# Optimization experiments

Measured on AMD Instinct MI355X. Metric: run time of the kernel, lower is better.

The kernel has to match this reference:

```python
import jax, jax.numpy as jnp
import numpy as np

B = 16384       # batch
H = 512         # hidden_size
OUT = 4         # output_size (== GRU input_size)
FF = 2048       # MLP hidden width
HORIZON = 5     # prediction_horizon


def setup_inputs() -> dict:
    key = jax.random.key(0)
    ks = jax.random.split(key, 12)
    s = 0.05
    f32 = jnp.float32
    return {
        "predicted_values": jax.random.normal(ks[0], (B, HORIZON, OUT), f32),
        "past_time_features": jax.random.normal(ks[1], (B, H), f32),
        # nn.GRU (single layer) params, PyTorch layout: (3H, in) / (3H, H), gate order r,z,n
        "w_ih": jax.random.normal(ks[2], (3 * H, OUT), f32) * s,
        "w_hh": jax.random.normal(ks[3], (3 * H, H), f32) * s,
        "b_ih": jax.random.normal(ks[4], (3 * H,), f32) * s,
        "b_hh": jax.random.normal(ks[5], (3 * H,), f32) * s,
        # hx_fc: Linear(2H -> H)
        "w_fc": jax.random.normal(ks[6], (H, 2 * H), f32) * s,
        "b_fc": jax.random.normal(ks[7], (H,), f32) * s,
        # mlp: Linear(H -> 2048), Linear(2048 -> OUT); Dropout is identity at eval
        "w1": jax.random.normal(ks[8], (FF, H), f32) * s,
        "b1": jax.random.normal(ks[9], (FF,), f32) * s,
        "w2": jax.random.normal(ks[10], (OUT, FF), f32) * s,
        "b2": jax.random.normal(ks[11], (OUT,), f32) * s,
    }


def _gru_cell(x, h, w_ih, w_hh, b_ih, b_hh):
    # PyTorch GRU cell: gates ordered (r, z, n)
    gi = x @ w_ih.T + b_ih          # [B, 3H]
    gh = h @ w_hh.T + b_hh          # [B, 3H]
    i_r, i_z, i_n = jnp.split(gi, 3, axis=-1)
    h_r, h_z, h_n = jnp.split(gh, 3, axis=-1)
    r = jax.nn.sigmoid(i_r + h_r)
    z = jax.nn.sigmoid(i_z + h_z)
    n = jnp.tanh(i_n + r * h_n)
    return (1.0 - z) * n + z * h


def reference(predicted_values, past_time_features, w_ih, w_hh, b_ih, b_hh,
              w_fc, b_fc, w1, b1, w2, b2):
    b = predicted_values.shape[0]
    xy = jnp.zeros((b, OUT), predicted_values.dtype)
    hx = past_time_features.reshape(b, H)
    outs = []
    for i in range(HORIZON):
        # length-2 sequence through the GRU: [xy, predicted_values[:, i]]
        h1 = _gru_cell(xy, hx, w_ih, w_hh, b_ih, b_hh)
        h2 = _gru_cell(predicted_values[:, i, :], h1, w_ih, w_hh, b_ih, b_hh)
        hcat = jnp.concatenate([h1, h2], axis=-1)        # [B, 2H]
        hx = hcat @ w_fc.T + b_fc                        # [B, H]
        # MLP: ReLU -> Linear -> (Dropout=identity) -> ReLU -> Linear
        d_xy = jax.nn.relu(jax.nn.relu(hx) @ w1.T + b1) @ w2.T + b2
        xy = xy + d_xy
        outs.append(xy)
    return jnp.stack(outs, axis=1)                       # [B, HORIZON, OUT]
```

## Files before the change

### kernel.cpp

```cpp
#include <hip/hip_runtime.h>
#include <hip/hip_bf16.h>
#include <cstdint>
#include <cstddef>

#define Bsz 16384
#define HORsz 5

using bf16_t = __hip_bfloat16;
typedef __bf16 bf16x8 __attribute__((ext_vector_type(8)));
typedef float f32x4 __attribute__((ext_vector_type(4)));

__device__ __forceinline__ void gld_lds16(const void* g, void* l) {
  __builtin_amdgcn_global_load_lds((__attribute__((address_space(1))) void*)g,
                                   (__attribute__((address_space(3))) void*)l,
                                   16, 0, 0);
}

__device__ __forceinline__ float sigm(float x) { return 1.f / (1.f + __expf(-x)); }
__device__ __forceinline__ float tanh_fast(float x) {
  x = fminf(fmaxf(x, -20.f), 20.f);
  float e = __expf(2.f * x);
  return (e - 1.f) / (e + 1.f);
}

__device__ __forceinline__ void swz(int b, int nbn, int& n, int& m) {
  const int x = b & 7;
  const int k = b >> 3;
  n = k % nbn;
  m = x + 8 * (k / nbn);
}

__device__ __forceinline__ size_t fl_off(int row, int col, int ca, int cofs) {
  return (size_t)((row >> 4) * ca + cofs + (col >> 5)) * 1024
       + (size_t)((((col >> 3) & 3) * 16 + (row & 15)) * 16 + (col & 7) * 2);
}

__global__ void __launch_bounds__(256) pack_fl(const float* __restrict__ src,
                                               char* __restrict__ dst,
                                               int C, int cs, int npieces) {
  const int p = blockIdx.x * 256 + threadIdx.x;
  if (p >= npieces) return;
  const int chunk = p >> 6, wi = p & 63;
  const int colgrp = wi >> 4, r15 = wi & 15;
  const int rowgrp = chunk >> cs, kg = chunk & ((1 << cs) - 1);
  const int row = rowgrp * 16 + r15;
  const int col = kg * 32 + colgrp * 8;
  const float* s = src + (size_t)row * C + col;
  bf16x8 v;
  #pragma unroll
  for (int j = 0; j < 8; ++j) v[j] = (__bf16)s[j];
  *(bf16x8*)(dst + (size_t)p * 16) = v;
}

__global__ void __launch_bounds__(256, 3) gru_fused4(
    const char* __restrict__ Afl, int ca,
    const char* __restrict__ Wfl,
    const float* __restrict__ x, int ldx,
    const float* __restrict__ w_ih, const float* __restrict__ b_ih,
    const float* __restrict__ b_hh,
    char* __restrict__ Ofl, int co, int kofs)
{
  __shared__ char smem[32768];
  const int t = threadIdx.x, w = t >> 6, lane = t & 63;
  int bn, bm;
  swz(blockIdx.x, 8, bn, bm);
  const int m0 = bm * 64;
  const int n0 = bn * 64;

  const char* gsrc[4];
  int loff[4];
  #pragma unroll
  for (int s = 0; s < 4; ++s) {
    const int idx = w * 4 + s;
    if (idx < 4) {
      gsrc[s] = Afl + (size_t)((m0 >> 4) + idx) * ca * 1024 + lane * 16;
    } else {
      const int c = idx - 4, g = c >> 2, cr = c & 3;
      gsrc[s] = Wfl + (size_t)(g * 32 + (n0 >> 4) + cr) * 16 * 1024 + lane * 16;
    }
    loff[s] = idx * 1024;
  }

  f32x4 acc[3][4];
  const f32x4 zero = {0.f, 0.f, 0.f, 0.f};
  #pragma unroll
  for (int g = 0; g < 3; ++g)
    #pragma unroll
    for (int i = 0; i < 4; ++i) acc[g][i] = zero;

  #pragma unroll
  for (int s = 0; s < 4; ++s)
    gld_lds16(gsrc[s], smem + loff[s]);

  #pragma unroll
  for (int kg = 0; kg < 16; ++kg) {
    __syncthreads();
    const char* cur = smem + (kg & 1) * 16384;
    if (kg + 1 < 16) {
      char* nxt = smem + ((kg + 1) & 1) * 16384;
      #pragma unroll
      for (int s = 0; s < 4; ++s)
        gld_lds16(gsrc[s] + (size_t)(kg + 1) * 1024, nxt + loff[s]);
    }
    bf16x8 af[4];
    #pragma unroll
    for (int i = 0; i < 4; ++i)
      af[i] = *(const bf16x8*)(cur + i * 1024 + lane * 16);
    #pragma unroll
    for (int g = 0; g < 3; ++g) {
      const bf16x8 bv = *(const bf16x8*)(cur + (4 + g * 4 + w) * 1024 + lane * 16);
      #pragma unroll
      for (int i = 0; i < 4; ++i)
        acc[g][i] = __builtin_amdgcn_mfma_f32_16x16x32_bf16(af[i], bv, acc[g][i], 0, 0, 0);
    }
  }

  const int lr = lane & 15, q4 = (lane >> 4) * 4;
  char* rep = smem + w * 2048;
  const int c = n0 + w * 16 + lr;
  const float4 wr  = *(const float4*)(w_ih + (size_t)c * 4);
  const float4 wz  = *(const float4*)(w_ih + (size_t)(c + 512) * 4);
  const float4 wnn = *(const float4*)(w_ih + (size_t)(c + 1024) * 4);
  const float bir = b_ih[c], biz = b_ih[c + 512], bin = b_ih[c + 1024];
  const float bhr = b_hh[c], bhz = b_hh[c + 512], bhn = b_hh[c + 1024];
  const int wbase = ((lr >> 3) * 16 + q4) * 16 + (lr & 7) * 2;
  #pragma unroll
  for (int i = 0; i < 4; ++i) {
    #pragma unroll
    for (int r4 = 0; r4 < 4; ++r4) {
      const int row = m0 + i * 16 + q4 + r4;
      const float4 xv = *(const float4*)(x + (size_t)row * ldx);
      const float gir = bir + xv.x * wr.x  + xv.y * wr.y  + xv.z * wr.z  + xv.w * wr.w;
      const float giz = biz + xv.x * wz.x  + xv.y * wz.y  + xv.z * wz.z  + xv.w * wz.w;
      const float gin = bin + xv.x * wnn.x + xv.y * wnn.y + xv.z * wnn.z + xv.w * wnn.w;
      const float rr = sigm(gir + acc[0][i][r4] + bhr);
      const float zz = sigm(giz + acc[1][i][r4] + bhz);
      const float nn = tanh_fast(gin + rr * (acc[2][i][r4] + bhn));
      const float hp = (float)*(const __bf16*)(Afl + fl_off(row, c, ca, 0));
      *(__bf16*)(rep + i * 512 + wbase + r4 * 16) = (__bf16)((1.f - zz) * nn + zz * hp);
    }
  }
  const int rg0 = m0 >> 4;
  const int cg = kofs + (n0 >> 5) + (w >> 1);
  const int half = (w & 1) * 512;
  #pragma unroll
  for (int i = 0; i < 4; ++i) {
    const uint2 v = *(const uint2*)(rep + i * 512 + lane * 8);
    *(uint2*)(Ofl + ((size_t)(rg0 + i) * co + cg) * 1024 + half + lane * 8) = v;
  }
}

template <int NKG, int NJ, int MODE>
__global__ void __launch_bounds__(256, 4) gemm_fl5(
    const char* __restrict__ Afl,
    const char* __restrict__ Bfl, int nbn,
    const float* __restrict__ bias,
    char* __restrict__ O1, char* __restrict__ O2, int co,
    const float* __restrict__ w2, float* __restrict__ dxy)
{
  constexpr int NCH = 8 + 2 * NJ;
  constexpr int NS = NCH / 4;
  constexpr int BUFB = NCH * 1024;
  __shared__ char smem[2 * BUFB];
  const int t = threadIdx.x, w = t >> 6, lane = t & 63;
  int bn, bm;
  swz(blockIdx.x, nbn, bn, bm);
  const int m0 = bm * 128, n0 = bn * (NJ * 32);
  const int wm = (w >> 1) * 64, wn = (w & 1) * (NJ * 16);

  const char* gsrc[NS];
  int loff[NS];
  #pragma unroll
  for (int s = 0; s < NS; ++s) {
    const int idx = w * NS + s;
    if (idx < 8) gsrc[s] = Afl + (size_t)((m0 >> 4) + idx) * NKG * 1024 + lane * 16;
    else         gsrc[s] = Bfl + (size_t)((n0 >> 4) + idx - 8) * NKG * 1024 + lane * 16;
    loff[s] = idx * 1024;
  }

  f32x4 acc[4][NJ];
  const f32x4 zero = {0.f, 0.f, 0.f, 0.f};
  #pragma unroll
  for (int i = 0; i < 4; ++i)
    #pragma unroll
    for (int j = 0; j < NJ; ++j) acc[i][j] = zero;

  #pragma unroll
  for (int s = 0; s < NS; ++s)
    gld_lds16(gsrc[s], smem + loff[s]);

  #pragma unroll
  for (int kg = 0; kg < NKG; ++kg) {
    __syncthreads();
    const char* cur = smem + (kg & 1) * BUFB;
    if (kg + 1 < NKG) {
      char* nxt = smem + ((kg + 1) & 1) * BUFB;
      #pragma unroll
      for (int s = 0; s < NS; ++s)
        gld_lds16(gsrc[s] + (size_t)(kg + 1) * 1024, nxt + loff[s]);
    }
    bf16x8 af[4], bv[NJ];
    #pragma unroll
    for (int i = 0; i < 4; ++i)
      af[i] = *(const bf16x8*)(cur + ((wm >> 4) + i) * 1024 + lane * 16);
    #pragma unroll
    for (int j = 0; j < NJ; ++j)
      bv[j] = *(const bf16x8*)(cur + (8 + (wn >> 4) + j) * 1024 + lane * 16);
    #pragma unroll
    for (int i = 0; i < 4; ++i)
      #pragma unroll
      for (int j = 0; j < NJ; ++j)
        acc[i][j] = __builtin_amdgcn_mfma_f32_16x16x32_bf16(af[i], bv[j], acc[i][j], 0, 0, 0);
  }

  const int lr = lane & 15, q4 = (lane >> 4) * 4;
  if (MODE == 2) {
    char* rep = smem + w * (NJ / 2) * 1024;
    const int rgb = (m0 >> 4) + (wm >> 4);
    const int cgb = (n0 >> 5) + (wn >> 5);
    for (int i = 0; i < 4; ++i) {
      #pragma unroll
      for (int j = 0; j < NJ; ++j) {
        const int col = n0 + wn + j * 16 + lr;
        const float bvv = bias[col];
        const int wbase = (((j & 1) * 2 + (lr >> 3)) * 16 + q4) * 16 + (lr & 7) * 2;
        #pragma unroll
        for (int r = 0; r < 4; ++r) {
          const float v = acc[i][j][r] + bvv;
          *(__bf16*)(rep + (j >> 1) * 1024 + wbase + r * 16) = (__bf16)v;
        }
      }
      #pragma unroll
      for (int jc = 0; jc < NJ / 2; ++jc) {
        const bf16x8 v = *(const bf16x8*)(rep + jc * 1024 + lane * 16);
        const size_t cb = ((size_t)(rgb + i) * co + cgb + jc) * 1024 + lane * 16;
        *(bf16x8*)(O1 + cb) = v;
        bf16x8 vr;
        #pragma unroll
        for (int e = 0; e < 8; ++e) vr[e] = (__bf16)fmaxf((float)v[e], 0.f);
        *(bf16x8*)(O2 + cb) = vr;
      }
    }
  } else {
    const int slice = bn * 2 + (w & 1);
    #pragma unroll
    for (int i = 0; i < 4; ++i) {
      float v[4][4];
      #pragma unroll
      for (int r = 0; r < 4; ++r)
        #pragma unroll
        for (int o = 0; o < 4; ++o) v[r][o] = 0.f;
      #pragma unroll
      for (int j = 0; j < NJ; ++j) {
        const int col = n0 + wn + j * 16 + lr;
        const float bvv = bias[col];
        const float w20 = w2[col], w21 = w2[2048 + col], w22 = w2[4096 + col], w23 = w2[6144 + col];
        #pragma unroll
        for (int r = 0; r < 4; ++r) {
          const float pv = fmaxf(acc[i][j][r] + bvv, 0.f);
          v[r][0] += pv * w20; v[r][1] += pv * w21; v[r][2] += pv * w22; v[r][3] += pv * w23;
        }
      }
      #pragma unroll
      for (int m = 1; m <= 8; m <<= 1)
        #pragma unroll
        for (int r = 0; r < 4; ++r)
          #pragma unroll
          for (int o = 0; o < 4; ++o) v[r][o] += __shfl_xor(v[r][o], m);
      if (lr == 0) {
        #pragma unroll
        for (int r = 0; r < 4; ++r) {
          const int row = m0 + wm + i * 16 + q4 + r;
          float4 vv = make_float4(v[r][0], v[r][1], v[r][2], v[r][3]);
          *(float4*)(dxy + ((size_t)slice * Bsz + row) * 4) = vv;
        }
      }
    }
  }
}

__global__ void __launch_bounds__(256) finalize(
    const float* __restrict__ dxy, const float* __restrict__ b2,
    float* __restrict__ xy, float* __restrict__ out, int istep)
{
  const int b = blockIdx.x * 256 + threadIdx.x;
  float4 s = *(const float4*)b2;
  #pragma unroll 8
  for (int sl = 0; sl < 32; ++sl) {
    const float4 d = *(const float4*)(dxy + ((size_t)sl * Bsz + b) * 4);
    s.x += d.x; s.y += d.y; s.z += d.z; s.w += d.w;
  }
  float4 xv = *(const float4*)(xy + (size_t)b * 4);
  xv.x += s.x; xv.y += s.y; xv.z += s.z; xv.w += s.w;
  *(float4*)(xy + (size_t)b * 4) = xv;
  *(float4*)(out + (size_t)b * 20 + istep * 4) = xv;
}

extern "C" void kernel_launch(void* const* d_in, const int* in_sizes, int n_in,
                              void* d_out, int out_size, void* d_ws, size_t ws_size,
                              hipStream_t stream)
{
  const float* pv   = (const float*)d_in[0];
  const float* ptf  = (const float*)d_in[1];
  const float* w_ih = (const float*)d_in[2];
  const float* w_hh = (const float*)d_in[3];
  const float* b_ih = (const float*)d_in[4];
  const float* b_hh = (const float*)d_in[5];
  const float* w_fc = (const float*)d_in[6];
  const float* b_fc = (const float*)d_in[7];
  const float* w1   = (const float*)d_in[8];
  const float* b1   = (const float*)d_in[9];
  const float* w2   = (const float*)d_in[10];
  const float* b2   = (const float*)d_in[11];
  float* out = (float*)d_out;

  char* p = (char*)d_ws;
  auto carve = [&](size_t bytes) {
    char* r = p;
    p += (bytes + 255) & ~(size_t)255;
    return r;
  };
  char*  hxF   = carve((size_t)Bsz * 512 * 2);
  char*  hxrF  = carve((size_t)Bsz * 512 * 2);
  char*  hcatF = carve((size_t)Bsz * 1024 * 2);
  float* dxy   = (float*)carve((size_t)32 * Bsz * 4 * 4);
  float* xy    = (float*)carve((size_t)Bsz * 4 * 4);
  char*  whhF  = carve((size_t)1536 * 512 * 2);
  char*  wfcF  = carve((size_t)512 * 1024 * 2);
  char*  w1F   = carve((size_t)2048 * 512 * 2);

  pack_fl<<<(1536 * 512 / 8 + 255) / 256, 256, 0, stream>>>(w_hh, whhF, 512, 4, 1536 * 512 / 8);
  pack_fl<<<(512 * 1024 / 8 + 255) / 256, 256, 0, stream>>>(w_fc, wfcF, 1024, 5, 512 * 1024 / 8);
  pack_fl<<<(2048 * 512 / 8 + 255) / 256, 256, 0, stream>>>(w1, w1F, 512, 4, 2048 * 512 / 8);
  pack_fl<<<(Bsz * 512 / 8 + 255) / 256, 256, 0, stream>>>(ptf, hxF, 512, 4, Bsz * 512 / 8);
  hipMemsetAsync(xy, 0, (size_t)Bsz * 4 * 4, stream);

  for (int i = 0; i < HORsz; ++i) {
    gru_fused4<<<2048, 256, 0, stream>>>(
        hxF, 16, whhF, xy, 4, w_ih, b_ih, b_hh, hcatF, 32, 0);
    gru_fused4<<<2048, 256, 0, stream>>>(
        hcatF, 32, whhF, pv + i * 4, HORsz * 4, w_ih, b_ih, b_hh, hcatF, 32, 16);
    gemm_fl5<32, 2, 2><<<1024, 256, 0, stream>>>(
        hcatF, wfcF, 8, b_fc, hxF, hxrF, 16, nullptr, nullptr);
    gemm_fl5<16, 4, 3><<<2048, 256, 0, stream>>>(
        hxrF, w1F, 16, b1, nullptr, nullptr, 0, w2, dxy);
    finalize<<<Bsz / 256, 256, 0, stream>>>(dxy, b2, xy, out, i);
  }
}
```

Before: 869.9 us.

## Triple-buffer LDS loads with explicit vmcnt waits and MFMA priority

```diff
diff --git a/kernel.cpp b/kernel.cpp
--- a/kernel.cpp
+++ b/kernel.cpp
@@ -14,6 +14,14 @@
   __builtin_amdgcn_global_load_lds((__attribute__((address_space(1))) void*)g,
                                    (__attribute__((address_space(3))) void*)l,
                                    16, 0, 0);
+}
+
+template <int N>
+__device__ __forceinline__ void wait_vmcnt() {
+  if constexpr (N == 0)      asm volatile("s_waitcnt vmcnt(0)" ::: "memory");
+  else if constexpr (N == 3) asm volatile("s_waitcnt vmcnt(3)" ::: "memory");
+  else if constexpr (N == 4) asm volatile("s_waitcnt vmcnt(4)" ::: "memory");
+  else static_assert(N == 0 || N == 3 || N == 4, "unsupported vmcnt");
 }
 
 __device__ __forceinline__ float sigm(float x) { return 1.f / (1.f + __expf(-x)); }
@@ -60,7 +68,7 @@
     const float* __restrict__ b_hh,
     char* __restrict__ Ofl, int co, int kofs)
 {
-  __shared__ char smem[32768];
+  __shared__ char smem[49152];
   const int t = threadIdx.x, w = t >> 6, lane = t & 63;
   int bn, bm;
   swz(blockIdx.x, 8, bn, bm);
@@ -91,29 +99,40 @@
   #pragma unroll
   for (int s = 0; s < 4; ++s)
     gld_lds16(gsrc[s], smem + loff[s]);
+  #pragma unroll
+  for (int s = 0; s < 4; ++s)
+    gld_lds16(gsrc[s] + 1024, smem + 16384 + loff[s]);
 
   #pragma unroll
   for (int kg = 0; kg < 16; ++kg) {
-    __syncthreads();
-    const char* cur = smem + (kg & 1) * 16384;
-    if (kg + 1 < 16) {
-      char* nxt = smem + ((kg + 1) & 1) * 16384;
+    if (kg + 1 < 16) wait_vmcnt<4>();
+    else             wait_vmcnt<0>();
+    __builtin_amdgcn_s_barrier();
+    __builtin_amdgcn_sched_barrier(0);
+    const char* cur = smem + (kg % 3) * 16384;
+    if (kg + 2 < 16) {
+      char* nxt = smem + ((kg + 2) % 3) * 16384;
       #pragma unroll
       for (int s = 0; s < 4; ++s)
-        gld_lds16(gsrc[s] + (size_t)(kg + 1) * 1024, nxt + loff[s]);
+        gld_lds16(gsrc[s] + (size_t)(kg + 2) * 1024, nxt + loff[s]);
     }
     bf16x8 af[4];
     #pragma unroll
     for (int i = 0; i < 4; ++i)
       af[i] = *(const bf16x8*)(cur + i * 1024 + lane * 16);
-    #pragma unroll
-    for (int g = 0; g < 3; ++g) {
-      const bf16x8 bv = *(const bf16x8*)(cur + (4 + g * 4 + w) * 1024 + lane * 16);
+    bf16x8 bvv[3];
+    #pragma unroll
+    for (int g = 0; g < 3; ++g)
+      bvv[g] = *(const bf16x8*)(cur + (4 + g * 4 + w) * 1024 + lane * 16);
+    __builtin_amdgcn_s_setprio(1);
+    #pragma unroll
+    for (int g = 0; g < 3; ++g)
       #pragma unroll
       for (int i = 0; i < 4; ++i)
-        acc[g][i] = __builtin_amdgcn_mfma_f32_16x16x32_bf16(af[i], bv, acc[g][i], 0, 0, 0);
-    }
-  }
+        acc[g][i] = __builtin_amdgcn_mfma_f32_16x16x32_bf16(af[i], bvv[g], acc[g][i], 0, 0, 0);
+    __builtin_amdgcn_s_setprio(0);
+  }
+  __syncthreads();
 
   const int lr = lane & 15, q4 = (lane >> 4) * 4;
   char* rep = smem + w * 2048;
@@ -161,7 +180,7 @@
   constexpr int NCH = 8 + 2 * NJ;
   constexpr int NS = NCH / 4;
   constexpr int BUFB = NCH * 1024;
-  __shared__ char smem[2 * BUFB];
+  __shared__ char smem[3 * BUFB];
   const int t = threadIdx.x, w = t >> 6, lane = t & 63;
   int bn, bm;
   swz(blockIdx.x, nbn, bn, bm);
@@ -188,16 +207,22 @@
   #pragma unroll
   for (int s = 0; s < NS; ++s)
     gld_lds16(gsrc[s], smem + loff[s]);
+  #pragma unroll
+  for (int s = 0; s < NS; ++s)
+    gld_lds16(gsrc[s] + 1024, smem + BUFB + loff[s]);
 
   #pragma unroll
   for (int kg = 0; kg < NKG; ++kg) {
-    __syncthreads();
-    const char* cur = smem + (kg & 1) * BUFB;
-    if (kg + 1 < NKG) {
-      char* nxt = smem + ((kg + 1) & 1) * BUFB;
+    if (kg + 1 < NKG) wait_vmcnt<NS>();
+    else              wait_vmcnt<0>();
+    __builtin_amdgcn_s_barrier();
+    __builtin_amdgcn_sched_barrier(0);
+    const char* cur = smem + (kg % 3) * BUFB;
+    if (kg + 2 < NKG) {
+      char* nxt = smem + ((kg + 2) % 3) * BUFB;
       #pragma unroll
       for (int s = 0; s < NS; ++s)
-        gld_lds16(gsrc[s] + (size_t)(kg + 1) * 1024, nxt + loff[s]);
+        gld_lds16(gsrc[s] + (size_t)(kg + 2) * 1024, nxt + loff[s]);
     }
     bf16x8 af[4], bv[NJ];
     #pragma unroll
@@ -206,12 +231,15 @@
     #pragma unroll
     for (int j = 0; j < NJ; ++j)
       bv[j] = *(const bf16x8*)(cur + (8 + (wn >> 4) + j) * 1024 + lane * 16);
+    __builtin_amdgcn_s_setprio(1);
     #pragma unroll
     for (int i = 0; i < 4; ++i)
       #pragma unroll
       for (int j = 0; j < NJ; ++j)
         acc[i][j] = __builtin_amdgcn_mfma_f32_16x16x32_bf16(af[i], bv[j], acc[i][j], 0, 0, 0);
-  }
+    __builtin_amdgcn_s_setprio(0);
+  }
+  if (MODE == 2) __syncthreads();
 
   const int lr = lane & 15, q4 = (lane >> 4) * 4;
   if (MODE == 2) {
```

Result: slower. 925.6 us (+6.4%).

## Load MFMA operands directly from global memory instead of LDS double-buffering

Applied to the files above, without the earlier changes.

```diff
diff --git a/kernel.cpp b/kernel.cpp
--- a/kernel.cpp
+++ b/kernel.cpp
@@ -9,12 +9,6 @@
 using bf16_t = __hip_bfloat16;
 typedef __bf16 bf16x8 __attribute__((ext_vector_type(8)));
 typedef float f32x4 __attribute__((ext_vector_type(4)));
-
-__device__ __forceinline__ void gld_lds16(const void* g, void* l) {
-  __builtin_amdgcn_global_load_lds((__attribute__((address_space(1))) void*)g,
-                                   (__attribute__((address_space(3))) void*)l,
-                                   16, 0, 0);
-}
 
 __device__ __forceinline__ float sigm(float x) { return 1.f / (1.f + __expf(-x)); }
 __device__ __forceinline__ float tanh_fast(float x) {
@@ -60,26 +54,21 @@
     const float* __restrict__ b_hh,
     char* __restrict__ Ofl, int co, int kofs)
 {
-  __shared__ char smem[32768];
+  __shared__ char rep_s[8192];
   const int t = threadIdx.x, w = t >> 6, lane = t & 63;
   int bn, bm;
   swz(blockIdx.x, 8, bn, bm);
   const int m0 = bm * 64;
   const int n0 = bn * 64;
 
-  const char* gsrc[4];
-  int loff[4];
-  #pragma unroll
-  for (int s = 0; s < 4; ++s) {
-    const int idx = w * 4 + s;
-    if (idx < 4) {
-      gsrc[s] = Afl + (size_t)((m0 >> 4) + idx) * ca * 1024 + lane * 16;
-    } else {
-      const int c = idx - 4, g = c >> 2, cr = c & 3;
-      gsrc[s] = Wfl + (size_t)(g * 32 + (n0 >> 4) + cr) * 16 * 1024 + lane * 16;
-    }
-    loff[s] = idx * 1024;
-  }
+  const char* aptr[4];
+  #pragma unroll
+  for (int i = 0; i < 4; ++i)
+    aptr[i] = Afl + (size_t)((m0 >> 4) + i) * ca * 1024 + lane * 16;
+  const char* wptr[3];
+  #pragma unroll
+  for (int g = 0; g < 3; ++g)
+    wptr[g] = Wfl + (size_t)(g * 32 + (n0 >> 4) + w) * 16 * 1024 + lane * 16;
 
   f32x4 acc[3][4];
   const f32x4 zero = {0.f, 0.f, 0.f, 0.f};
@@ -89,34 +78,24 @@
     for (int i = 0; i < 4; ++i) acc[g][i] = zero;
 
   #pragma unroll
-  for (int s = 0; s < 4; ++s)
-    gld_lds16(gsrc[s], smem + loff[s]);
-
-  #pragma unroll
   for (int kg = 0; kg < 16; ++kg) {
-    __syncthreads();
-    const char* cur = smem + (kg & 1) * 16384;
-    if (kg + 1 < 16) {
-      char* nxt = smem + ((kg + 1) & 1) * 16384;
-      #pragma unroll
-      for (int s = 0; s < 4; ++s)
-        gld_lds16(gsrc[s] + (size_t)(kg + 1) * 1024, nxt + loff[s]);
-    }
     bf16x8 af[4];
     #pragma unroll
     for (int i = 0; i < 4; ++i)
-      af[i] = *(const bf16x8*)(cur + i * 1024 + lane * 16);
-    #pragma unroll
-    for (int g = 0; g < 3; ++g) {
-      const bf16x8 bv = *(const bf16x8*)(cur + (4 + g * 4 + w) * 1024 + lane * 16);
+      af[i] = *(const bf16x8*)(aptr[i] + (size_t)kg * 1024);
+    bf16x8 bvv[3];
+    #pragma unroll
+    for (int g = 0; g < 3; ++g)
+      bvv[g] = *(const bf16x8*)(wptr[g] + (size_t)kg * 1024);
+    #pragma unroll
+    for (int g = 0; g < 3; ++g)
       #pragma unroll
       for (int i = 0; i < 4; ++i)
-        acc[g][i] = __builtin_amdgcn_mfma_f32_16x16x32_bf16(af[i], bv, acc[g][i], 0, 0, 0);
-    }
+        acc[g][i] = __builtin_amdgcn_mfma_f32_16x16x32_bf16(af[i], bvv[g], acc[g][i], 0, 0, 0);
   }
 
   const int lr = lane & 15, q4 = (lane >> 4) * 4;
-  char* rep = smem + w * 2048;
+  char* rep = rep_s + w * 2048;
   const int c = n0 + w * 16 + lr;
   const float4 wr  = *(const float4*)(w_ih + (size_t)c * 4);
   const float4 wz  = *(const float4*)(w_ih + (size_t)(c + 512) * 4);
@@ -158,25 +137,20 @@
     char* __restrict__ O1, char* __restrict__ O2, int co,
     const float* __restrict__ w2, float* __restrict__ dxy)
 {
-  constexpr int NCH = 8 + 2 * NJ;
-  constexpr int NS = NCH / 4;
-  constexpr int BUFB = NCH * 1024;
-  __shared__ char smem[2 * BUFB];
   const int t = threadIdx.x, w = t >> 6, lane = t & 63;
   int bn, bm;
   swz(blockIdx.x, nbn, bn, bm);
   const int m0 = bm * 128, n0 = bn * (NJ * 32);
   const int wm = (w >> 1) * 64, wn = (w & 1) * (NJ * 16);
 
-  const char* gsrc[NS];
-  int loff[NS];
-  #pragma unroll
-  for (int s = 0; s < NS; ++s) {
-    const int idx = w * NS + s;
-    if (idx < 8) gsrc[s] = Afl + (size_t)((m0 >> 4) + idx) * NKG * 1024 + lane * 16;
-    else         gsrc[s] = Bfl + (size_t)((n0 >> 4) + idx - 8) * NKG * 1024 + lane * 16;
-    loff[s] = idx * 1024;
-  }
+  const char* aptr[4];
+  #pragma unroll
+  for (int i = 0; i < 4; ++i)
+    aptr[i] = Afl + (size_t)((m0 >> 4) + (wm >> 4) + i) * NKG * 1024 + lane * 16;
+  const char* bptr[NJ];
+  #pragma unroll
+  for (int j = 0; j < NJ; ++j)
+    bptr[j] = Bfl + (size_t)((n0 >> 4) + (wn >> 4) + j) * NKG * 1024 + lane * 16;
 
   f32x4 acc[4][NJ];
   const f32x4 zero = {0.f, 0.f, 0.f, 0.f};
@@ -186,26 +160,14 @@
     for (int j = 0; j < NJ; ++j) acc[i][j] = zero;
 
   #pragma unroll
-  for (int s = 0; s < NS; ++s)
-    gld_lds16(gsrc[s], smem + loff[s]);
-
-  #pragma unroll
   for (int kg = 0; kg < NKG; ++kg) {
-    __syncthreads();
-    const char* cur = smem + (kg & 1) * BUFB;
-    if (kg + 1 < NKG) {
-      char* nxt = smem + ((kg + 1) & 1) * BUFB;
-      #pragma unroll
-      for (int s = 0; s < NS; ++s)
-        gld_lds16(gsrc[s] + (size_t)(kg + 1) * 1024, nxt + loff[s]);
-    }
     bf16x8 af[4], bv[NJ];
     #pragma unroll
     for (int i = 0; i < 4; ++i)
-      af[i] = *(const bf16x8*)(cur + ((wm >> 4) + i) * 1024 + lane * 16);
+      af[i] = *(const bf16x8*)(aptr[i] + (size_t)kg * 1024);
     #pragma unroll
     for (int j = 0; j < NJ; ++j)
-      bv[j] = *(const bf16x8*)(cur + (8 + (wn >> 4) + j) * 1024 + lane * 16);
+      bv[j] = *(const bf16x8*)(bptr[j] + (size_t)kg * 1024);
     #pragma unroll
     for (int i = 0; i < 4; ++i)
       #pragma unroll
@@ -214,10 +176,12 @@
   }
 
   const int lr = lane & 15, q4 = (lane >> 4) * 4;
-  if (MODE == 2) {
-    char* rep = smem + w * (NJ / 2) * 1024;
+  if constexpr (MODE == 2) {
+    __shared__ char rep_s[(NJ / 2) * 4 * 1024];
+    char* rep = rep_s + w * (NJ / 2) * 1024;
     const int rgb = (m0 >> 4) + (wm >> 4);
     const int cgb = (n0 >> 5) + (wn >> 5);
+    #pragma unroll
     for (int i = 0; i < 4; ++i) {
       #pragma unroll
       for (int j = 0; j < NJ; ++j) {
```

New measurement: 1.149 ms. 32.1% more time.

## Replace MLP GEMM with dedicated 256x256-tile triple-buffered mlp8 kernel

Applied to the files above, without the earlier changes.

```diff
diff --git a/kernel.cpp b/kernel.cpp
--- a/kernel.cpp
+++ b/kernel.cpp
@@ -14,6 +14,13 @@
   __builtin_amdgcn_global_load_lds((__attribute__((address_space(1))) void*)g,
                                    (__attribute__((address_space(3))) void*)l,
                                    16, 0, 0);
+}
+
+template <int N>
+__device__ __forceinline__ void wait_vmcnt() {
+  if constexpr (N == 0)      asm volatile("s_waitcnt vmcnt(0)" ::: "memory");
+  else if constexpr (N == 4) asm volatile("s_waitcnt vmcnt(4)" ::: "memory");
+  else static_assert(N == 0 || N == 4, "unsupported vmcnt");
 }
 
 __device__ __forceinline__ float sigm(float x) { return 1.f / (1.f + __expf(-x)); }
@@ -241,39 +248,152 @@
         *(bf16x8*)(O2 + cb) = vr;
       }
     }
-  } else {
-    const int slice = bn * 2 + (w & 1);
-    #pragma unroll
-    for (int i = 0; i < 4; ++i) {
-      float v[4][4];
+  }
+}
+
+__global__ void __launch_bounds__(512, 2) mlp8(
+    const char* __restrict__ Afl,
+    const char* __restrict__ Bfl,
+    const float* __restrict__ bias,
+    const float* __restrict__ w2,
+    float* __restrict__ dxy)
+{
+  __shared__ char smem[3 * 32768];
+  const int t = threadIdx.x, w = t >> 6, lane = t & 63;
+  const int wr = w >> 2, wc = w & 3;
+  int bn, bm;
+  swz(blockIdx.x, 8, bn, bm);
+  const int m0 = bm * 256, n0 = bn * 256;
+
+  const char* gsrc[4];
+  int loff[4];
+  #pragma unroll
+  for (int s = 0; s < 4; ++s) {
+    const int idx = w * 4 + s;
+    if (idx < 16) {
+      gsrc[s] = Afl + (size_t)((m0 >> 4) + idx) * 16 * 1024 + lane * 16;
+      loff[s] = idx * 1024;
+    } else {
+      gsrc[s] = Bfl + (size_t)((n0 >> 4) + idx - 16) * 16 * 1024 + lane * 16;
+      loff[s] = 16384 + (idx - 16) * 1024;
+    }
+  }
+
+  f32x4 acc[8][4];
+  const f32x4 zero = {0.f, 0.f, 0.f, 0.f};
+  #pragma unroll
+  for (int i = 0; i < 8; ++i)
+    #pragma unroll
+    for (int j = 0; j < 4; ++j) acc[i][j] = zero;
+
+  #pragma unroll
+  for (int s = 0; s < 4; ++s)
+    gld_lds16(gsrc[s], smem + loff[s]);
+  #pragma unroll
+  for (int s = 0; s < 4; ++s)
+    gld_lds16(gsrc[s] + 1024, smem + 32768 + loff[s]);
+
+  #pragma unroll
+  for (int T = 0; T < 14; ++T) {
+    wait_vmcnt<4>();
+    __builtin_amdgcn_s_barrier();
+    __builtin_amdgcn_sched_barrier(0);
+    const char* cur = smem + (T % 3) * 32768;
+    char* nxt = smem + ((T + 2) % 3) * 32768;
+    gld_lds16(gsrc[0] + (size_t)(T + 2) * 1024, nxt + loff[0]);
+    gld_lds16(gsrc[1] + (size_t)(T + 2) * 1024, nxt + loff[1]);
+    bf16x8 bv[4], af[4];
+    #pragma unroll
+    for (int j = 0; j < 4; ++j)
+      bv[j] = *(const bf16x8*)(cur + 16384 + (wc * 4 + j) * 1024 + lane * 16);
+    #pragma unroll
+    for (int i = 0; i < 4; ++i)
+      af[i] = *(const bf16x8*)(cur + (wr * 8 + i) * 1024 + lane * 16);
+    __builtin_amdgcn_s_setprio(1);
+    #pragma unroll
+    for (int i = 0; i < 4; ++i)
+      #pragma unroll
+      for (int j = 0; j < 4; ++j)
+        acc[i][j] = __builtin_amdgcn_mfma_f32_16x16x32_bf16(af[i], bv[j], acc[i][j], 0, 0, 0);
+    __builtin_amdgcn_s_setprio(0);
+    gld_lds16(gsrc[2] + (size_t)(T + 2) * 1024, nxt + loff[2]);
+    gld_lds16(gsrc[3] + (size_t)(T + 2) * 1024, nxt + loff[3]);
+    #pragma unroll
+    for (int i = 0; i < 4; ++i)
+      af[i] = *(const bf16x8*)(cur + (wr * 8 + 4 + i) * 1024 + lane * 16);
+    __builtin_amdgcn_s_setprio(1);
+    #pragma unroll
+    for (int i = 0; i < 4; ++i)
+      #pragma unroll
+      for (int j = 0; j < 4; ++j)
+        acc[4 + i][j] = __builtin_amdgcn_mfma_f32_16x16x32_bf16(af[i], bv[j], acc[4 + i][j], 0, 0, 0);
+    __builtin_amdgcn_s_setprio(0);
+  }
+  #pragma unroll
+  for (int T = 14; T < 16; ++T) {
+    if (T == 14) wait_vmcnt<4>();
+    else         wait_vmcnt<0>();
+    __builtin_amdgcn_s_barrier();
+    __builtin_amdgcn_sched_barrier(0);
+    const char* cur = smem + (T % 3) * 32768;
+    bf16x8 bv[4], af[4];
+    #pragma unroll
+    for (int j = 0; j < 4; ++j)
+      bv[j] = *(const bf16x8*)(cur + 16384 + (wc * 4 + j) * 1024 + lane * 16);
+    #pragma unroll
+    for (int i = 0; i < 4; ++i)
+      af[i] = *(const bf16x8*)(cur + (wr * 8 + i) * 1024 + lane * 16);
+    __builtin_amdgcn_s_setprio(1);
+    #pragma unroll
+    for (int i = 0; i < 4; ++i)
+      #pragma unroll
+      for (int j = 0; j < 4; ++j)
+        acc[i][j] = __builtin_amdgcn_mfma_f32_16x16x32_bf16(af[i], bv[j], acc[i][j], 0, 0, 0);
+    __builtin_amdgcn_s_setprio(0);
+    #pragma unroll
+    for (int i = 0; i < 4; ++i)
+      af[i] = *(const bf16x8*)(cur + (wr * 8 + 4 + i) * 1024 + lane * 16);
+    __builtin_amdgcn_s_setprio(1);
+    #pragma unroll
+    for (int i = 0; i < 4; ++i)
+      #pragma unroll
+      for (int j = 0; j < 4; ++j)
+        acc[4 + i][j] = __builtin_amdgcn_mfma_f32_16x16x32_bf16(af[i], bv[j], acc[4 + i][j], 0, 0, 0);
+    __builtin_amdgcn_s_setprio(0);
+  }
+
+  const int lr = lane & 15, q4 = (lane >> 4) * 4;
+  const int slice = bn * 4 + wc;
+  #pragma unroll
+  for (int i = 0; i < 8; ++i) {
+    float v[4][4];
+    #pragma unroll
+    for (int r = 0; r < 4; ++r)
+      #pragma unroll
+      for (int o = 0; o < 4; ++o) v[r][o] = 0.f;
+    #pragma unroll
+    for (int j = 0; j < 4; ++j) {
+      const int col = n0 + wc * 64 + j * 16 + lr;
+      const float bvv = bias[col];
+      const float w20 = w2[col], w21 = w2[2048 + col], w22 = w2[4096 + col], w23 = w2[6144 + col];
+      #pragma unroll
+      for (int r = 0; r < 4; ++r) {
+        const float pv = fmaxf(acc[i][j][r] + bvv, 0.f);
+        v[r][0] += pv * w20; v[r][1] += pv * w21; v[r][2] += pv * w22; v[r][3] += pv * w23;
+      }
+    }
+    #pragma unroll
+    for (int m = 1; m <= 8; m <<= 1)
       #pragma unroll
       for (int r = 0; r < 4; ++r)
         #pragma unroll
-        for (int o = 0; o < 4; ++o) v[r][o] = 0.f;
-      #pragma unroll
-      for (int j = 0; j < NJ; ++j) {
-        const int col = n0 + wn + j * 16 + lr;
-        const float bvv = bias[col];
-        const float w20 = w2[col], w21 = w2[2048 + col], w22 = w2[4096 + col], w23 = w2[6144 + col];
-        #pragma unroll
-        for (int r = 0; r < 4; ++r) {
-          const float pv = fmaxf(acc[i][j][r] + bvv, 0.f);
-          v[r][0] += pv * w20; v[r][1] += pv * w21; v[r][2] += pv * w22; v[r][3] += pv * w23;
-        }
-      }
-      #pragma unroll
-      for (int m = 1; m <= 8; m <<= 1)
-        #pragma unroll
-        for (int r = 0; r < 4; ++r)
-          #pragma unroll
-          for (int o = 0; o < 4; ++o) v[r][o] += __shfl_xor(v[r][o], m);
-      if (lr == 0) {
-        #pragma unroll
-        for (int r = 0; r < 4; ++r) {
-          const int row = m0 + wm + i * 16 + q4 + r;
-          float4 vv = make_float4(v[r][0], v[r][1], v[r][2], v[r][3]);
-          *(float4*)(dxy + ((size_t)slice * Bsz + row) * 4) = vv;
-        }
+        for (int o = 0; o < 4; ++o) v[r][o] += __shfl_xor(v[r][o], m);
+    if (lr == 0) {
+      #pragma unroll
+      for (int r = 0; r < 4; ++r) {
+        const int row = m0 + wr * 128 + i * 16 + q4 + r;
+        float4 vv = make_float4(v[r][0], v[r][1], v[r][2], v[r][3]);
+        *(float4*)(dxy + ((size_t)slice * Bsz + row) * 4) = vv;
       }
     }
   }
@@ -342,8 +462,7 @@
         hcatF, 32, whhF, pv + i * 4, HORsz * 4, w_ih, b_ih, b_hh, hcatF, 32, 16);
     gemm_fl5<32, 2, 2><<<1024, 256, 0, stream>>>(
         hcatF, wfcF, 8, b_fc, hxF, hxrF, 16, nullptr, nullptr);
-    gemm_fl5<16, 4, 3><<<2048, 256, 0, stream>>>(
-        hxrF, w1F, 16, b1, nullptr, nullptr, 0, w2, dxy);
+    mlp8<<<512, 512, 0, stream>>>(hxrF, w1F, b1, w2, dxy);
     finalize<<<Bsz / 256, 256, 0, stream>>>(dxy, b2, xy, out, i);
   }
 }
```

Measured after the change: 907.5 us. 1.04x slower.
